# Performance work log

Measured on AMD Instinct MI355X. Metric: run time of the kernel, lower is better.

Reference implementation:

```python
import jax, jax.numpy as jnp
import numpy as np

SCALES = (0, 1, 2, 3)
SIGMA_NSQ = 2.0
SIGMA_MAX_INV = 4.0 / (255.0 * 255.0)
GAIN_LIMIT = 100.0  # NEG=False
EPS = 1e-10


def gaussian_kernel_2d(N):
    sigma = N / 5.0
    x = jnp.arange(N, dtype=jnp.float32) - (N - 1) / 2.0
    g = jnp.exp(-(x * x) / (2.0 * sigma * sigma))
    k = jnp.outer(g, g)
    return (k / jnp.sum(k))[None, None]  # [1,1,N,N]


def reflect_pad(x, p):
    return jnp.pad(x, ((0, 0), (0, 0), (p, p), (p, p)), mode='reflect')


def conv2d(x, w, stride=1, groups=1):
    return jax.lax.conv_general_dilated(
        x, w, (stride, stride), 'VALID',
        dimension_numbers=('NCHW', 'OIHW', 'NCHW'),
        feature_group_count=groups)


def vif_num_den(ref, dist):
    ref = ref - 128.0
    dist = dist - 128.0
    h, w = ref.shape[-2], ref.shape[-1]
    nums, dens = [], []
    for scale in SCALES:
        N = 2 ** (4 - scale) + 1
        win = gaussian_kernel_2d(N)
        p = (N - 1) // 2
        if scale > 0:
            h, w = h // 2, w // 2
            ref = conv2d(reflect_pad(ref, p), win, stride=2)[:, :, :h, :w]
            dist = conv2d(reflect_pad(dist, p), win, stride=2)[:, :, :h, :w]
        win5 = jnp.tile(win, (5, 1, 1, 1))  # grouped conv, 5 channels
        inp = jnp.concatenate([ref, dist, ref * ref, dist * dist, ref * dist], axis=1)
        out = conv2d(reflect_pad(inp, p), win5, groups=5)  # [b,5,h,w]
        mu1, mu2, s1, s2, s12 = [out[:, i:i + 1] for i in range(5)]
        s1 = jax.nn.relu(s1 - mu1 * mu1)
        s2 = jax.nn.relu(s2 - mu2 * mu2)
        s12 = s12 - mu1 * mu2
        g = s12 / (s1 + EPS)
        sv = s2 - g * s12
        m1 = s1 < EPS
        g = jnp.where(m1, 0.0, g)
        sv = jnp.where(m1, s2, sv)
        s1 = jnp.where(m1, 0.0, s1)
        m2 = s2 < EPS
        g = jnp.where(m2, 0.0, g)
        sv = jnp.where(m2, 0.0, sv)
        sv = jnp.where(g < 0.0, s2, sv)
        g = jax.nn.relu(g)
        sv = jnp.where(sv <= EPS, EPS, sv)
        g = jnp.minimum(g, GAIN_LIMIT)
        num_ar = jnp.log2(1.0 + g * g * s1 / (sv + SIGMA_NSQ))
        den_ar = jnp.log2(1.0 + s1 / SIGMA_NSQ)
        num_ar = jnp.where(s12 < 0.0, 0.0, num_ar)
        m3 = s1 < SIGMA_NSQ
        num_ar = jnp.where(m3, 1.0 - s2 * SIGMA_MAX_INV, num_ar)
        den_ar = jnp.where(m3, 1.0, den_ar)
        nums.append(jnp.sum(num_ar, axis=(-1, -2, -3)))
        dens.append(jnp.sum(den_ar, axis=(-1, -2, -3)))
    return jnp.stack(nums, axis=-1), jnp.stack(dens, axis=-1)


def setup_inputs() -> dict:
    key = jax.random.key(0)
    k1, k2 = jax.random.split(key)
    shape = (4, 1, 1080, 1920)
    ref = jax.random.uniform(k1, shape, dtype=jnp.float32) * 255.0
    dist = jax.random.uniform(k2, shape, dtype=jnp.float32) * 255.0
    return {"ref": ref, "dist": dist}


def reference(ref, dist):
    num, den = vif_num_den(ref, dist)
    return num / den  # VIF features per scale, shape [b, 4]
```

## Files before the change

### kernel.cpp

```cpp
#include <hip/hip_runtime.h>
#include <math.h>

#define VIF_EPS       1e-10f
#define SIGMA_NSQ     2.0f
#define SIGMA_MAX_INV (4.0f / (255.0f * 255.0f))
#define GAIN_LIMIT    100.0f

typedef float v2f __attribute__((ext_vector_type(2)));
typedef float v4f __attribute__((ext_vector_type(4)));

static __device__ __forceinline__ v2f splat2(float s) {
    v2f v; v.x = s; v.y = s; return v;
}

__device__ __forceinline__ int reflect_idx(int i, int n) {
    i = (i < 0) ? -i : i;
    i = (i >= n) ? (2 * n - 2 - i) : i;
    return i;
}

template <int N>
__device__ __forceinline__ void fill_weights_global(float* gw) {
    const float sigma = (float)N / 5.0f;
    const float denom = 2.0f * sigma * sigma;
    float tmp[N];
    float s = 0.0f;
    for (int i = 0; i < N; ++i) {
        float x = (float)i - (float)(N - 1) * 0.5f;
        float g = expf(-(x * x) / denom);
        tmp[i] = g;
        s += g;
    }
    for (int i = 0; i < N; ++i) gw[i] = tmp[i] / s;
}

__global__ __launch_bounds__(64) void init_weights_kernel(float* __restrict__ gw) {
    const int tid = threadIdx.x;
    if (tid == 0) fill_weights_global<17>(gw + 0);
    else if (tid == 1) fill_weights_global<9>(gw + 17);
    else if (tid == 2) fill_weights_global<5>(gw + 26);
    else if (tid == 3) fill_weights_global<3>(gw + 31);
}

__host__ __device__ constexpr int w_off(int N) {
    return (N == 17) ? 0 : (N == 9) ? 17 : (N == 5) ? 26 : 31;
}

constexpr int tile_w(int N) { return (256 - (N - 1)) & ~3; }

template <int N>
struct alignas(16) StatsSmem {
    v2f   a[8][256];
    v2f   bq[8][256];
    float c[8][256];
};
template <int N>
struct alignas(16) DownSmem {
    v2f vb[8][252];
};
struct alignas(16) Stats3Smem {
    union {
        StatsSmem<3> planes;
        v2f vb3[10][481];
    } u2;
    v2f patch[10][240];
};

template <int N, bool FROM_PATCH>
__device__ __forceinline__ void stats_body(
    StatsSmem<N>& sm, const float* __restrict__ refp, const float* __restrict__ distp,
    const v2f* __restrict__ patch,
    const float* __restrict__ gw,
    int h, int w, float shift, double2* __restrict__ partial,
    int sy, int sx, int bx, int b) {
    constexpr int P   = (N - 1) / 2;
    constexpr int TW  = tile_w(N);
    constexpr int TH  = 8;
    constexpr int LR  = TH + 2 * P;
    constexpr int XG4 = TW / 4;
    constexpr int NT  = TH * XG4;
    constexpr int REPS = (NT + 255) / 256;

    const int tid = threadIdx.x;
    const int ytile = bx % sy;
    const int xtile = bx / sy;
    const int x0 = xtile * TW;
    const int y0 = ytile * TH;

    float wr[N];
#pragma unroll
    for (int j = 0; j < N; ++j) wr[j] = gw[j];

    {
        const int cc = tid;
        const int gx = reflect_idx(x0 + cc - P, w);

        v2f accA[TH], accB[TH];
        float accC[TH];
#pragma unroll
        for (int t = 0; t < TH; ++t) {
            accA[t] = splat2(0.f);
            accB[t] = splat2(0.f);
            accC[t] = 0.f;
        }

        auto acc_push = [&](int i, float r, float d) {
            v2f rd; rd.x = r; rd.y = d;
            v2f sq = rd * rd;
            float x = r * d;
#pragma unroll
            for (int t = 0; t < TH; ++t) {
                const int j = i - t;
                if (j >= 0 && j < N) {
                    const float wj = wr[j];
                    accA[t] += splat2(wj) * rd;
                    accB[t] += splat2(wj) * sq;
                    accC[t] += wj * x;
                }
            }
        };

        if constexpr (FROM_PATCH) {
#pragma unroll
            for (int i = 0; i < LR; ++i) {
                v2f pv = patch[i * 240 + gx];
                acc_push(i, pv.x, pv.y);
            }
        } else {
            const float* rbase = refp  + (size_t)b * h * w;
            const float* dbase = distp + (size_t)b * h * w;

            float rrow[LR], drow[LR];
            const int rowlo = y0 - P;
            if (rowlo >= 0 && rowlo + LR <= h) {
                unsigned voff = (unsigned)(rowlo * w + gx) * 4u;
                const unsigned vstep = (unsigned)w * 4u;
#pragma unroll
                for (int i = 0; i < LR; ++i) {
                    rrow[i] = *(const float*)((const char*)rbase + voff);
                    drow[i] = *(const float*)((const char*)dbase + voff);
                    voff += vstep;
                }
            } else {
#pragma unroll
                for (int i = 0; i < LR; ++i) {
                    const int gy = reflect_idx(rowlo + i, h);
                    const size_t o = (size_t)gy * w + gx;
                    rrow[i] = rbase[o];
                    drow[i] = dbase[o];
                }
            }
#pragma unroll
            for (int i = 0; i < LR; ++i)
                acc_push(i, rrow[i] - shift, drow[i] - shift);
        }
#pragma unroll
        for (int t = 0; t < TH; ++t) {
            sm.a[t][cc]  = accA[t];
            sm.bq[t][cc] = accB[t];
            sm.c[t][cc]  = accC[t];
        }
    }
    __syncthreads();

    float num_v = 0.f, den_v = 0.f;
    {
        constexpr int WC  = N + 3;
        constexpr int F4C = (WC + 3) / 4;
#pragma unroll
        for (int rep = 0; rep < REPS; ++rep) {
            const int task = tid + 256 * rep;
            if (task < NT) {
                const int row = task / XG4;
                const int xg  = task - row * XG4;

                v2f muA[4], muB[4];
                float muC[4];
#pragma unroll
                for (int q = 0; q < 4; ++q) {
                    muA[q] = splat2(0.f);
                    muB[q] = splat2(0.f);
                    muC[q] = 0.f;
                }

                const v4f* A4 = (const v4f*)&sm.a[row][xg * 4];
                const v4f* B4 = (const v4f*)&sm.bq[row][xg * 4];
#pragma unroll
                for (int f = 0; f < WC / 2; ++f) {
                    v4f ta = A4[f];
                    v4f tb = B4[f];
#pragma unroll
                    for (int hlf = 0; hlf < 2; ++hlf) {
                        const int k = 2 * f + hlf;
                        v2f pa = hlf ? __builtin_shufflevector(ta, ta, 2, 3)
                                     : __builtin_shufflevector(ta, ta, 0, 1);
                        v2f pb = hlf ? __builtin_shufflevector(tb, tb, 2, 3)
                                     : __builtin_shufflevector(tb, tb, 0, 1);
#pragma unroll
                        for (int q = 0; q < 4; ++q) {
                            const int j = k - q;
                            if (j >= 0 && j < N) {
                                const float wj = wr[j];
                                muA[q] += splat2(wj) * pa;
                                muB[q] += splat2(wj) * pb;
                            }
                        }
                    }
                }
                {
                    const v4f* C4 = (const v4f*)&sm.c[row][xg * 4];
#pragma unroll
                    for (int f = 0; f < F4C; ++f) {
                        v4f t = C4[f];
#pragma unroll
                        for (int e = 0; e < 4; ++e) {
                            const int k = 4 * f + e;
                            const float x = (e == 0) ? t.x : (e == 1) ? t.y
                                          : (e == 2) ? t.z : t.w;
#pragma unroll
                            for (int q = 0; q < 4; ++q) {
                                const int j = k - q;
                                if (j >= 0 && j < N) muC[q] += wr[j] * x;
                            }
                        }
                    }
                }

                const int gy = y0 + row;
#pragma unroll
                for (int q = 0; q < 4; ++q) {
                    int gx = x0 + xg * 4 + q;
                    if (gx < w && gy < h) {
                        float mu1 = muA[q].x, mu2 = muA[q].y;
                        float s1  = fmaxf(0.f, muB[q].x - mu1 * mu1);
                        float s2  = fmaxf(0.f, muB[q].y - mu2 * mu2);
                        float s12 = muC[q] - mu1 * mu2;

                        float g  = s12 / (s1 + VIF_EPS);
                        float sv = s2 - g * s12;
                        if (s1 < VIF_EPS) { g = 0.f; sv = s2; s1 = 0.f; }
                        if (s2 < VIF_EPS) { g = 0.f; sv = 0.f; }
                        if (g  < 0.f)     { sv = s2; g = 0.f; }
                        if (sv <= VIF_EPS) sv = VIF_EPS;
                        g = fminf(g, GAIN_LIMIT);

                        float num_ar = __log2f(1.f + g * g * s1 / (sv + SIGMA_NSQ));
                        float den_ar = __log2f(1.f + s1 / SIGMA_NSQ);
                        if (s12 < 0.f) num_ar = 0.f;
                        if (s1 < SIGMA_NSQ) { num_ar = 1.f - s2 * SIGMA_MAX_INV; den_ar = 1.f; }
                        num_v += num_ar;
                        den_v += den_ar;
                    }
                }
            }
        }
    }

#pragma unroll
    for (int off = 32; off > 0; off >>= 1) {
        num_v += __shfl_down(num_v, off);
        den_v += __shfl_down(den_v, off);
    }
    __syncthreads();
    float* rs = reinterpret_cast<float*>(&sm);
    const int wid = tid >> 6, lane = tid & 63;
    if (lane == 0) { rs[wid] = num_v; rs[4 + wid] = den_v; }
    __syncthreads();
    if (tid == 0) {
        float ns = rs[0] + rs[1] + rs[2] + rs[3];
        float ds = rs[4] + rs[5] + rs[6] + rs[7];
        partial[(size_t)b * (sy * sx) + bx] = make_double2((double)ns, (double)ds);
    }
}

template <int N>
__device__ __forceinline__ void down_body(
    DownSmem<N>& sm, const float* __restrict__ rin, const float* __restrict__ din,
    const float* __restrict__ gw,
    float* __restrict__ rout, float* __restrict__ dout,
    int h, int w, int h2, int w2, float shift, int dgx, int bx, int b) {
    constexpr int P   = (N - 1) / 2;
    constexpr int TOW = 120, TOH = 8;
    constexpr int IC  = 2 * (TOW - 1) + N;
    constexpr int NR  = 2 * (TOH - 1) + N;
    constexpr int XG4 = TOW / 4;
    constexpr int WL  = N + 6;

    float wr[N];
#pragma unroll
    for (int j = 0; j < N; ++j) wr[j] = gw[j];

    const int tid = threadIdx.x;
    const int xt  = bx % dgx;
    const int yt  = bx / dgx;
    const int x0  = xt * TOW;
    const int y0  = yt * TOH;

    if (tid < IC) {
        const int gx = reflect_idx(2 * x0 - P + tid, w);
        const int rowlo = 2 * y0 - P;
        const float* rbase = rin + (size_t)b * h * w;
        const float* dbase = din + (size_t)b * h * w;

        float rr[NR], dd[NR];
        const bool interior = (rowlo >= 0) && (rowlo + NR <= h);
        if (interior) {
            unsigned voff = (unsigned)(rowlo * w + gx) * 4u;
            const unsigned vstep = (unsigned)w * 4u;
#pragma unroll
            for (int i = 0; i < NR; ++i) {
                rr[i] = *(const float*)((const char*)rbase + voff);
                dd[i] = *(const float*)((const char*)dbase + voff);
                voff += vstep;
            }
        } else {
#pragma unroll
            for (int i = 0; i < NR; ++i) {
                const int gy = reflect_idx(rowlo + i, h);
                const size_t o = (size_t)gy * w + gx;
                rr[i] = rbase[o];
                dd[i] = dbase[o];
            }
        }

        v2f acc[TOH];
#pragma unroll
        for (int t = 0; t < TOH; ++t) acc[t] = splat2(0.f);
#pragma unroll
        for (int i = 0; i < NR; ++i) {
            v2f x; x.x = rr[i] - shift; x.y = dd[i] - shift;
#pragma unroll
            for (int t = 0; t < TOH; ++t) {
                const int j = i - 2 * t;
                if (j >= 0 && j < N) acc[t] += splat2(wr[j]) * x;
            }
        }
#pragma unroll
        for (int t = 0; t < TOH; ++t) sm.vb[t][tid] = acc[t];
    }
    __syncthreads();

    if (tid < TOH * XG4) {
        const int row = tid / XG4;
        const int xg  = tid - row * XG4;

        v2f o[4];
#pragma unroll
        for (int q = 0; q < 4; ++q) o[q] = splat2(0.f);

        const v4f* s4 = (const v4f*)&sm.vb[row][8 * xg];
#pragma unroll
        for (int f = 0; f < (WL + 1) / 2; ++f) {
            v4f t = s4[f];
#pragma unroll
            for (int hlf = 0; hlf < 2; ++hlf) {
                const int k = 2 * f + hlf;
                v2f p = hlf ? __builtin_shufflevector(t, t, 2, 3)
                            : __builtin_shufflevector(t, t, 0, 1);
#pragma unroll
                for (int q = 0; q < 4; ++q) {
                    const int j = k - 2 * q;
                    if (j >= 0 && j < N) o[q] += splat2(wr[j]) * p;
                }
            }
        }
        const int gy = y0 + row;
        if (gy < h2) {
            float* rp = rout + (size_t)b * h2 * w2 + (size_t)gy * w2 + x0 + 4 * xg;
            float* dp = dout + (size_t)b * h2 * w2 + (size_t)gy * w2 + x0 + 4 * xg;
            *(float4*)rp = make_float4(o[0].x, o[1].x, o[2].x, o[3].x);
            *(float4*)dp = make_float4(o[0].y, o[1].y, o[2].y, o[3].y);
        }
    }
}

template <int NS, int ND>
__global__ __launch_bounds__(256) void fused_kernel(
    const float* __restrict__ sref, const float* __restrict__ sdist,
    const float* __restrict__ gw,
    int sh, int sw, float sshift, double2* __restrict__ partial, int sy, int sx,
    float* __restrict__ drout, float* __restrict__ ddout,
    int dh2, int dw2, int dgx, int nStats) {
    __shared__ union {
        StatsSmem<NS> s;
        DownSmem<ND>  d;
    } u;
    const int bx = blockIdx.x;
    const int b  = blockIdx.z;
    if (bx < nStats)
        stats_body<NS, false>(u.s, sref, sdist, nullptr, gw + w_off(NS), sh, sw,
                              sshift, partial, sy, sx, bx, b);
    else
        down_body<ND>(u.d, sref, sdist, gw + w_off(ND), drout, ddout,
                      sh, sw, dh2, dw2, sshift, dgx, bx - nStats, b);
}

__device__ __forceinline__ void build_l3_patch(
    v2f* __restrict__ vb3 , v2f* __restrict__ patch ,
    const float* __restrict__ r2, const float* __restrict__ d2,
    const float* __restrict__ gw3, int y0, int b) {
    constexpr int H2v = 270, W2v = 480, H3v = 135;
    const int tid = threadIdx.x;
    const float w0 = gw3[0], w1 = gw3[1], w2 = gw3[2];
    const float* rb = r2 + (size_t)b * H2v * W2v;
    const float* db = d2 + (size_t)b * H2v * W2v;

#pragma unroll
    for (int rep = 0; rep < 2; ++rep) {
        const int t = tid + 256 * rep;
        if (t < 481) {
            const int c2 = reflect_idx(t - 1, W2v);
#pragma unroll
            for (int py = 0; py < 10; ++py) {
                const int y3  = reflect_idx(y0 - 1 + py, H3v);
                const int r0  = reflect_idx(2 * y3 - 1, H2v);
                const int r1  = 2 * y3;
                const int r2i = 2 * y3 + 1;
                v2f m = splat2(0.f);
                v2f x;
                x.x = rb[(size_t)r0 * W2v + c2];  x.y = db[(size_t)r0 * W2v + c2];
                m += splat2(w0) * x;
                x.x = rb[(size_t)r1 * W2v + c2];  x.y = db[(size_t)r1 * W2v + c2];
                m += splat2(w1) * x;
                x.x = rb[(size_t)r2i * W2v + c2]; x.y = db[(size_t)r2i * W2v + c2];
                m += splat2(w2) * x;
                vb3[py * 481 + t] = m;
            }
        }
    }
    __syncthreads();
#pragma unroll
    for (int rep = 0; rep < 10; ++rep) {
        const int idx = tid + 256 * rep;
        if (idx < 2400) {
            const int py = idx / 240;
            const int x3 = idx - py * 240;
            v2f o = splat2(0.f);
            o += splat2(w0) * vb3[py * 481 + 2 * x3 + 0];
            o += splat2(w1) * vb3[py * 481 + 2 * x3 + 1];
            o += splat2(w2) * vb3[py * 481 + 2 * x3 + 2];
            patch[py * 240 + x3] = o;
        }
    }
    __syncthreads();
}

__global__ __launch_bounds__(256) void level23_kernel(
    const float* __restrict__ ref2, const float* __restrict__ dist2,
    const float* __restrict__ gw,
    double2* __restrict__ p2, double2* __restrict__ p3) {
    __shared__ union {
        StatsSmem<5> s5;
        Stats3Smem   s3;
    } u;
    const int bx = blockIdx.x;
    const int b  = blockIdx.z;

    if (bx < 68) {
        stats_body<5, false>(u.s5, ref2, dist2, nullptr, gw + w_off(5),
                             270, 480, 0.f, p2, 34, 2, bx, b);
    } else {
        const int bx3 = bx - 68;
        build_l3_patch(&u.s3.u2.vb3[0][0], &u.s3.patch[0][0],
                       ref2, dist2, gw + w_off(3), bx3 * 8, b);
        stats_body<3, true>(u.s3.u2.planes, nullptr, nullptr, &u.s3.patch[0][0],
                            gw + w_off(3), 135, 240, 0.f, p3, 17, 1, bx3, b);
    }
}

__global__ __launch_bounds__(256) void reduce_kernel(
    const double2* __restrict__ part, float* __restrict__ out,
    int4 bases, int4 counts) {
    __shared__ double sn[4], sd[4];
    const int s = blockIdx.x & 3;
    const int b = blockIdx.x >> 2;
    const int base = (&bases.x)[s];
    const int cnt  = (&counts.x)[s];
    const double2* p = part + base + (size_t)b * cnt;

    double ns = 0.0, ds = 0.0;
    for (int i = threadIdx.x; i < cnt; i += 256) {
        double2 v = p[i];
        ns += v.x;
        ds += v.y;
    }
#pragma unroll
    for (int off = 32; off > 0; off >>= 1) {
        ns += __shfl_down(ns, off);
        ds += __shfl_down(ds, off);
    }
    const int wid = threadIdx.x >> 6, lane = threadIdx.x & 63;
    if (lane == 0) { sn[wid] = ns; sd[wid] = ds; }
    __syncthreads();
    if (threadIdx.x == 0) {
        double Nv = sn[0] + sn[1] + sn[2] + sn[3];
        double Dv = sd[0] + sd[1] + sd[2] + sd[3];
        out[b * 4 + s] = (float)(Nv / Dv);
    }
}

extern "C" void kernel_launch(void* const* d_in, const int* in_sizes, int n_in,
                              void* d_out, int out_size, void* d_ws, size_t ws_size,
                              hipStream_t stream) {
    const float* ref  = (const float*)d_in[0];
    const float* dist = (const float*)d_in[1];
    float* out = (float*)d_out;

    const int B = 4;
    const int H0 = 1080, W0 = 1920;
    const int H1 = 540,  W1 = 960;
    const int H2 = 270,  W2 = 480;

    char*  ws  = (char*)d_ws;
    size_t off = 0;
    auto alloc = [&](size_t bytes) -> void* {
        void* p = ws + off;
        off += (bytes + 255) & ~(size_t)255;
        return p;
    };
    float* gw    = (float*)alloc(34 * sizeof(float));
    float* ref1  = (float*)alloc((size_t)B * H1 * W1 * 4);
    float* dist1 = (float*)alloc((size_t)B * H1 * W1 * 4);
    float* ref2  = (float*)alloc((size_t)B * H2 * W2 * 4);
    float* dist2 = (float*)alloc((size_t)B * H2 * W2 * 4);

    const int sx0 = (W0 + tile_w(17) - 1) / tile_w(17), sy0 = (H0 + 7) / 8;
    const int sx1 = (W1 + tile_w(9)  - 1) / tile_w(9),  sy1 = (H1 + 7) / 8;
    const int n0 = sx0 * sy0;
    const int n1 = sx1 * sy1;
    const int n2 = 68;
    const int n3 = 17;

    const int dgx1 = W1 / 120, nD1 = dgx1 * ((H1 + 7) / 8);
    const int dgx2 = W2 / 120, nD2 = dgx2 * ((H2 + 7) / 8);

    double2* part = (double2*)alloc((size_t)B * (n0 + n1 + n2 + n3) * sizeof(double2));
    double2* p0 = part;
    double2* p1 = p0 + (size_t)B * n0;
    double2* p2 = p1 + (size_t)B * n1;
    double2* p3 = p2 + (size_t)B * n2;

    dim3 blk(256);

    init_weights_kernel<<<1, 64, 0, stream>>>(gw);

    fused_kernel<17, 9><<<dim3(n0 + nD1, 1, B), blk, 0, stream>>>(
        ref, dist, gw, H0, W0, 128.0f, p0, sy0, sx0,
        ref1, dist1, H1, W1, dgx1, n0);

    fused_kernel<9, 5><<<dim3(n1 + nD2, 1, B), blk, 0, stream>>>(
        ref1, dist1, gw, H1, W1, 0.0f, p1, sy1, sx1,
        ref2, dist2, H2, W2, dgx2, n1);

    level23_kernel<<<dim3(n2 + n3, 1, B), blk, 0, stream>>>(
        ref2, dist2, gw, p2, p3);

    reduce_kernel<<<16, 256, 0, stream>>>(
        part, out,
        make_int4(0, B * n0, B * (n0 + n1), B * (n0 + n1 + n2)),
        make_int4(n0, n1, n2, n3));
}
```

Measured before the change: 166.4 us.

## Fuse downsampling into stats tiles, reusing the loaded rows for the strided conv

Drops the separate downsample blocks and computes the strided Gaussian downsample inside each stats tile. It reuses the vertical column data already loaded in registers and passes the horizontal pass through shared memory. This is meant to remove the second global read of each level's input and the extra blocks. In exchange it adds register pressure and a post-stats shared-memory stage to every stats block, and it relies on tile width and halo alignment lining up with the downsampled output coverage.

```diff
diff --git a/kernel.cpp b/kernel.cpp
--- a/kernel.cpp
+++ b/kernel.cpp
@@ -54,10 +54,6 @@
     v2f   bq[8][256];
     float c[8][256];
 };
-template <int N>
-struct alignas(16) DownSmem {
-    v2f vb[8][252];
-};
 struct alignas(16) Stats3Smem {
     union {
         StatsSmem<3> planes;
@@ -66,11 +62,12 @@
     v2f patch[10][240];
 };
 
-template <int N, bool FROM_PATCH>
+template <int N, bool FROM_PATCH, int DN>
 __device__ __forceinline__ void stats_body(
     StatsSmem<N>& sm, const float* __restrict__ refp, const float* __restrict__ distp,
     const v2f* __restrict__ patch,
-    const float* __restrict__ gw,
+    const float* __restrict__ gw, const float* __restrict__ gwd,
+    float* __restrict__ drout, float* __restrict__ ddout, int dh2, int dw2,
     int h, int w, float shift, double2* __restrict__ partial,
     int sy, int sx, int bx, int b) {
     constexpr int P   = (N - 1) / 2;
@@ -80,6 +77,7 @@
     constexpr int XG4 = TW / 4;
     constexpr int NT  = TH * XG4;
     constexpr int REPS = (NT + 255) / 256;
+    constexpr int OFF = (DN > 0) ? (N - 1) / 2 - (DN - 1) / 2 : 0;
 
     const int tid = threadIdx.x;
     const int ytile = bx % sy;
@@ -90,6 +88,18 @@
     float wr[N];
 #pragma unroll
     for (int j = 0; j < N; ++j) wr[j] = gw[j];
+
+    float wd[DN > 0 ? DN : 1];
+    if constexpr (DN > 0) {
+#pragma unroll
+        for (int j = 0; j < DN; ++j) wd[j] = gwd[j];
+    }
+
+    v2f dacc[4];
+    if constexpr (DN > 0) {
+#pragma unroll
+        for (int t = 0; t < 4; ++t) dacc[t] = splat2(0.f);
+    }
 
     {
         const int cc = tid;
@@ -116,6 +126,13 @@
                     accA[t] += splat2(wj) * rd;
                     accB[t] += splat2(wj) * sq;
                     accC[t] += wj * x;
+                }
+            }
+            if constexpr (DN > 0) {
+#pragma unroll
+                for (int t = 0; t < 4; ++t) {
+                    const int j = i - 2 * t - OFF;
+                    if (j >= 0 && j < DN) dacc[t] += splat2(wd[j]) * rd;
                 }
             }
         };
@@ -265,7 +282,39 @@
     float* rs = reinterpret_cast<float*>(&sm);
     const int wid = tid >> 6, lane = tid & 63;
     if (lane == 0) { rs[wid] = num_v; rs[4 + wid] = den_v; }
+    if constexpr (DN > 0) {
+        v2f* vbd = &sm.bq[0][0];
+#pragma unroll
+        for (int t = 0; t < 4; ++t) vbd[t * 256 + tid] = dacc[t];
+    }
     __syncthreads();
+
+    if constexpr (DN > 0) {
+        constexpr int XGD = TW / 8;
+        if (tid < 4 * XGD) {
+            const int row = tid / XGD;
+            const int xg  = tid - row * XGD;
+            const v2f* vrow = &sm.bq[0][0] + row * 256;
+            v2f o[4];
+#pragma unroll
+            for (int q = 0; q < 4; ++q) o[q] = splat2(0.f);
+#pragma unroll
+            for (int jc = 0; jc < DN; ++jc) {
+                const v2f wj = splat2(wd[jc]);
+#pragma unroll
+                for (int q = 0; q < 4; ++q)
+                    o[q] += wj * vrow[8 * xg + 2 * q + OFF + jc];
+            }
+            const int gy2 = (y0 >> 1) + row;
+            const int gx2 = (x0 >> 1) + 4 * xg;
+            if (gy2 < dh2 && gx2 < dw2) {
+                float* rp = drout + (size_t)b * dh2 * dw2 + (size_t)gy2 * dw2 + gx2;
+                float* dp = ddout + (size_t)b * dh2 * dw2 + (size_t)gy2 * dw2 + gx2;
+                *(float4*)rp = make_float4(o[0].x, o[1].x, o[2].x, o[3].x);
+                *(float4*)dp = make_float4(o[0].y, o[1].y, o[2].y, o[3].y);
+            }
+        }
+    }
     if (tid == 0) {
         float ns = rs[0] + rs[1] + rs[2] + rs[3];
         float ds = rs[4] + rs[5] + rs[6] + rs[7];
@@ -273,126 +322,18 @@
     }
 }
 
-template <int N>
-__device__ __forceinline__ void down_body(
-    DownSmem<N>& sm, const float* __restrict__ rin, const float* __restrict__ din,
-    const float* __restrict__ gw,
-    float* __restrict__ rout, float* __restrict__ dout,
-    int h, int w, int h2, int w2, float shift, int dgx, int bx, int b) {
-    constexpr int P   = (N - 1) / 2;
-    constexpr int TOW = 120, TOH = 8;
-    constexpr int IC  = 2 * (TOW - 1) + N;
-    constexpr int NR  = 2 * (TOH - 1) + N;
-    constexpr int XG4 = TOW / 4;
-    constexpr int WL  = N + 6;
-
-    float wr[N];
-#pragma unroll
-    for (int j = 0; j < N; ++j) wr[j] = gw[j];
-
-    const int tid = threadIdx.x;
-    const int xt  = bx % dgx;
-    const int yt  = bx / dgx;
-    const int x0  = xt * TOW;
-    const int y0  = yt * TOH;
-
-    if (tid < IC) {
-        const int gx = reflect_idx(2 * x0 - P + tid, w);
-        const int rowlo = 2 * y0 - P;
-        const float* rbase = rin + (size_t)b * h * w;
-        const float* dbase = din + (size_t)b * h * w;
-
-        float rr[NR], dd[NR];
-        const bool interior = (rowlo >= 0) && (rowlo + NR <= h);
-        if (interior) {
-            unsigned voff = (unsigned)(rowlo * w + gx) * 4u;
-            const unsigned vstep = (unsigned)w * 4u;
-#pragma unroll
-            for (int i = 0; i < NR; ++i) {
-                rr[i] = *(const float*)((const char*)rbase + voff);
-                dd[i] = *(const float*)((const char*)dbase + voff);
-                voff += vstep;
-            }
-        } else {
-#pragma unroll
-            for (int i = 0; i < NR; ++i) {
-                const int gy = reflect_idx(rowlo + i, h);
-                const size_t o = (size_t)gy * w + gx;
-                rr[i] = rbase[o];
-                dd[i] = dbase[o];
-            }
-        }
-
-        v2f acc[TOH];
-#pragma unroll
-        for (int t = 0; t < TOH; ++t) acc[t] = splat2(0.f);
-#pragma unroll
-        for (int i = 0; i < NR; ++i) {
-            v2f x; x.x = rr[i] - shift; x.y = dd[i] - shift;
-#pragma unroll
-            for (int t = 0; t < TOH; ++t) {
-                const int j = i - 2 * t;
-                if (j >= 0 && j < N) acc[t] += splat2(wr[j]) * x;
-            }
-        }
-#pragma unroll
-        for (int t = 0; t < TOH; ++t) sm.vb[t][tid] = acc[t];
-    }
-    __syncthreads();
-
-    if (tid < TOH * XG4) {
-        const int row = tid / XG4;
-        const int xg  = tid - row * XG4;
-
-        v2f o[4];
-#pragma unroll
-        for (int q = 0; q < 4; ++q) o[q] = splat2(0.f);
-
-        const v4f* s4 = (const v4f*)&sm.vb[row][8 * xg];
-#pragma unroll
-        for (int f = 0; f < (WL + 1) / 2; ++f) {
-            v4f t = s4[f];
-#pragma unroll
-            for (int hlf = 0; hlf < 2; ++hlf) {
-                const int k = 2 * f + hlf;
-                v2f p = hlf ? __builtin_shufflevector(t, t, 2, 3)
-                            : __builtin_shufflevector(t, t, 0, 1);
-#pragma unroll
-                for (int q = 0; q < 4; ++q) {
-                    const int j = k - 2 * q;
-                    if (j >= 0 && j < N) o[q] += splat2(wr[j]) * p;
-                }
-            }
-        }
-        const int gy = y0 + row;
-        if (gy < h2) {
-            float* rp = rout + (size_t)b * h2 * w2 + (size_t)gy * w2 + x0 + 4 * xg;
-            float* dp = dout + (size_t)b * h2 * w2 + (size_t)gy * w2 + x0 + 4 * xg;
-            *(float4*)rp = make_float4(o[0].x, o[1].x, o[2].x, o[3].x);
-            *(float4*)dp = make_float4(o[0].y, o[1].y, o[2].y, o[3].y);
-        }
-    }
-}
-
 template <int NS, int ND>
-__global__ __launch_bounds__(256) void fused_kernel(
+__global__ __launch_bounds__(256) void stats_down_kernel(
     const float* __restrict__ sref, const float* __restrict__ sdist,
     const float* __restrict__ gw,
     int sh, int sw, float sshift, double2* __restrict__ partial, int sy, int sx,
-    float* __restrict__ drout, float* __restrict__ ddout,
-    int dh2, int dw2, int dgx, int nStats) {
-    __shared__ union {
-        StatsSmem<NS> s;
-        DownSmem<ND>  d;
-    } u;
-    const int bx = blockIdx.x;
-    const int b  = blockIdx.z;
-    if (bx < nStats)
-        stats_body<NS, false>(u.s, sref, sdist, nullptr, gw + w_off(NS), sh, sw,
-                              sshift, partial, sy, sx, bx, b);
-    else
-        down_body<ND>(u.d, sref, sdist, gw + w_off(ND), drout, ddout,
-                      sh, sw, dh2, dw2, sshift, dgx, bx - nStats, b);
+    float* __restrict__ drout, float* __restrict__ ddout, int dh2, int dw2) {
+    __shared__ StatsSmem<NS> sm;
+    stats_body<NS, false, ND>(sm, sref, sdist, nullptr,
+                              gw + w_off(NS), gw + w_off(ND),
+                              drout, ddout, dh2, dw2,
+                              sh, sw, sshift, partial, sy, sx,
+                              blockIdx.x, blockIdx.z);
 }
 
 __device__ __forceinline__ void build_l3_patch(
@@ -457,14 +398,18 @@
     const int b  = blockIdx.z;
 
     if (bx < 68) {
-        stats_body<5, false>(u.s5, ref2, dist2, nullptr, gw + w_off(5),
-                             270, 480, 0.f, p2, 34, 2, bx, b);
+        stats_body<5, false, 0>(u.s5, ref2, dist2, nullptr,
+                                gw + w_off(5), nullptr,
+                                nullptr, nullptr, 0, 0,
+                                270, 480, 0.f, p2, 34, 2, bx, b);
     } else {
         const int bx3 = bx - 68;
         build_l3_patch(&u.s3.u2.vb3[0][0], &u.s3.patch[0][0],
                        ref2, dist2, gw + w_off(3), bx3 * 8, b);
-        stats_body<3, true>(u.s3.u2.planes, nullptr, nullptr, &u.s3.patch[0][0],
-                            gw + w_off(3), 135, 240, 0.f, p3, 17, 1, bx3, b);
+        stats_body<3, true, 0>(u.s3.u2.planes, nullptr, nullptr, &u.s3.patch[0][0],
+                               gw + w_off(3), nullptr,
+                               nullptr, nullptr, 0, 0,
+                               135, 240, 0.f, p3, 17, 1, bx3, b);
     }
 }
 
@@ -531,9 +476,6 @@
     const int n2 = 68;
     const int n3 = 17;
 
-    const int dgx1 = W1 / 120, nD1 = dgx1 * ((H1 + 7) / 8);
-    const int dgx2 = W2 / 120, nD2 = dgx2 * ((H2 + 7) / 8);
-
     double2* part = (double2*)alloc((size_t)B * (n0 + n1 + n2 + n3) * sizeof(double2));
     double2* p0 = part;
     double2* p1 = p0 + (size_t)B * n0;
@@ -544,13 +486,13 @@
 
     init_weights_kernel<<<1, 64, 0, stream>>>(gw);
 
-    fused_kernel<17, 9><<<dim3(n0 + nD1, 1, B), blk, 0, stream>>>(
+    stats_down_kernel<17, 9><<<dim3(n0, 1, B), blk, 0, stream>>>(
         ref, dist, gw, H0, W0, 128.0f, p0, sy0, sx0,
-        ref1, dist1, H1, W1, dgx1, n0);
-
-    fused_kernel<9, 5><<<dim3(n1 + nD2, 1, B), blk, 0, stream>>>(
+        ref1, dist1, H1, W1);
+
+    stats_down_kernel<9, 5><<<dim3(n1, 1, B), blk, 0, stream>>>(
         ref1, dist1, gw, H1, W1, 0.0f, p1, sy1, sx1,
-        ref2, dist2, H2, W2, dgx2, n1);
+        ref2, dist2, H2, W2);
 
     level23_kernel<<<dim3(n2 + n3, 1, B), blk, 0, stream>>>(
         ref2, dist2, gw, p2, p3);
```

Result: no change. 164.4 us (-1.2%).
